# Kernel optimization log

Hardware: AMD Instinct MI355X
Metric: run time of the kernel (lower is better)

Reference implementation:

```python
import jax, jax.numpy as jnp
import numpy as np


def setup_inputs() -> dict:
    key = jax.random.key(0)
    ks = jax.random.split(key, 12)
    B, D, H, T, K = 12288, 1024, 512, 12, 3
    s = 0.02  # weight init scale for numerical stability
    return {
        "x": jax.random.normal(ks[0], (B, D), jnp.float32),
        "Wp": jax.random.normal(ks[1], (H, D), jnp.float32) * s,
        "bp": jnp.zeros((H,), jnp.float32),
        "opW1": jax.random.normal(ks[2], (T, K, H, H), jnp.float32) * s,
        "opb1": jnp.zeros((T, K, H), jnp.float32),
        "opW2": jax.random.normal(ks[3], (T, K, H, H), jnp.float32) * s,
        "opb2": jnp.zeros((T, K, H), jnp.float32),
        "op_logits": jax.random.normal(ks[4], (T, K), jnp.float32) * 0.1,
        "id_emb": jax.random.normal(ks[5], (T, 4), jnp.float32),
        "rW1": jax.random.normal(ks[6], (H, H + 7), jnp.float32) * s,
        "rb1": jnp.zeros((H,), jnp.float32),
        "rW2": jax.random.normal(ks[7], (T + 1, H), jnp.float32) * s,
        "rb2": jnp.zeros((T + 1,), jnp.float32),
        "gW1": jax.random.normal(ks[8], (T, H, 7), jnp.float32) * s,
        "gb1": jnp.zeros((T, H), jnp.float32),
        "gW2": jax.random.normal(ks[9], (T, 2, H), jnp.float32) * s,
        "gb2": jnp.zeros((T, 2), jnp.float32),
        "phW": jax.random.normal(ks[10], (D, H), jnp.float32) * s,
        "phb": jnp.zeros((D,), jnp.float32),
        "noise": jax.random.normal(ks[11], (B, H), jnp.float32),
    }


def reference(x, Wp, bp, opW1, opb1, opW2, opb2, op_logits, id_emb,
              rW1, rb1, rW2, rb2, gW1, gb1, gW2, gb2, phW, phb, noise):
    T, K, H, _ = opW1.shape
    B = x.shape[0]
    g = B // T  # balanced deterministic routing: patch p -> temper p % T

    # input projection (patch_size == hidden_dim => patches == x_proj)
    xp = x @ Wp.T + bp                                   # [B, H]
    xg = xp.reshape(g, T, H).transpose(1, 0, 2)           # [T, g, H]

    # Temper.apply_operators: softmax-weighted sum of Linear-ReLU-Linear-ReLU ops
    w = jax.nn.softmax(op_logits, axis=-1)                # [T, K]
    h1 = jax.nn.relu(jnp.einsum('tgj,tkij->tkgi', xg, opW1) + opb1[:, :, None, :])
    h2 = jax.nn.relu(jnp.einsum('tkgj,tkij->tkgi', h1, opW2) + opb2[:, :, None, :])
    out = jnp.einsum('tk,tkgi->tgi', w, h2)               # [T, g, H]
    # freshness buffers start at 0 -> fresh-bonus branch inactive

    usage = w                                             # usage starts at 0, += w
    conflict = jnp.std(w, axis=-1, ddof=1)                # torch.std is unbiased
    plast_t = ((out - xg) ** 2).mean(axis=(1, 2))         # last_plasticity per temper

    # IntrinsicGrowthController.compute_intrinsic_signals (buffers at init values)
    ng = noise.reshape(g, T, H).transpose(1, 0, 2) * 0.01
    plasticity = (ng ** 2).mean(-1)                       # [T, g] ((out_noisy-out)^2)
    novelty = (xg ** 2).mean(-1)                          # input_mean == 0
    pred_err = ((out - xg) ** 2).mean(-1)
    up = usage / (usage.sum(-1, keepdims=True) + 1e-6)
    entropy = -(up * jnp.log(jnp.clip(up, 1e-6, None))).sum(-1)   # [T]
    sparsity = jnp.abs(out).mean(-1)
    reward_delta = -pred_err                              # moving avg starts at 0
    new_avg = 0.01 * pred_err.mean(-1)                    # updated moving avg
    reward_var = ((pred_err - new_avg[:, None]) ** 2).mean(-1)
    signals = jnp.stack([plasticity.mean(-1), novelty.mean(-1), pred_err.mean(-1),
                         entropy, sparsity.mean(-1), reward_delta.mean(-1),
                         reward_var], axis=-1)            # [T, 7]

    # growth controller MLP 7 -> H -> 2 (per temper)
    gc_h = jax.nn.relu(jnp.einsum('thj,tj->th', gW1, signals) + gb1)
    decision = jnp.einsum('toh,th->to', gW2, gc_h) + gb2  # [T, 2] (grow, prune)

    # enriched routing input: [out | id_embed(4) | novelty | conflict | plasticity]
    nov_e = jnp.broadcast_to(signals[:, 1][:, None, None], (T, g, 1))
    conf_e = jnp.broadcast_to(conflict[:, None, None], (T, g, 1))
    plas_e = jnp.broadcast_to(plast_t[:, None, None], (T, g, 1))
    ide = jnp.broadcast_to(id_emb[:, None, :], (T, g, id_emb.shape[1]))
    enriched = jnp.concatenate([out, ide, nov_e, conf_e, plas_e], axis=-1)  # [T,g,H+7]

    rh = jax.nn.relu(jnp.einsum('tgj,ij->tgi', enriched, rW1) + rb1)
    logits = jnp.einsum('tgj,ij->tgi', rh, rW2) + rb2     # [T, g, T+1]

    # scatter back to original patch order (inverse of the grouping reshape)
    out_full = out.transpose(1, 0, 2).reshape(B, H)
    logits_full = logits.transpose(1, 0, 2).reshape(B, T + 1)
    pred = out_full @ phW.T + phb                         # predictive head [B, D]
    return (out_full, logits_full, pred, decision)
```

## Files before the change

### kernel.cpp

```cpp
#include <hip/hip_runtime.h>

typedef unsigned short u16;
typedef float f32x4 __attribute__((ext_vector_type(4)));
typedef float f32x8 __attribute__((ext_vector_type(8)));
typedef u16   u16x4 __attribute__((ext_vector_type(4)));
typedef u16   u16x8 __attribute__((ext_vector_type(8)));
typedef __bf16 bf16x8 __attribute__((ext_vector_type(8)));

#define WS_W       0u
#define WS_BIASRH  512u
#define WS_WPB     25600u
#define WS_PHWB    1074176u
#define WS_RW1B    2122752u
#define WS_W1B     2647040u
#define WS_W2B     21521408u
#define WS_XPB     40395776u
#define WS_H1B     52978688u
#define WS_XBF     90727424u
#define WS_OUTB    90727424u
#define WS_RHB     103310336u

#define OUT_LG   6291456
#define OUT_PRED 6451200
#define OUT_DEC  19034112

__device__ __forceinline__ u16 f2bf(float f) {
    unsigned u = __builtin_bit_cast(unsigned, f);
    return (u16)((u + 0x7FFFu + ((u >> 16) & 1u)) >> 16);
}
__device__ __forceinline__ float bf2f(u16 h) {
    return __builtin_bit_cast(float, (unsigned)h << 16);
}

typedef __attribute__((address_space(1))) void* gas1p;
typedef __attribute__((address_space(3))) void* las3p;
__device__ __forceinline__ void gload16(const u16* g, u16* l) {
    __builtin_amdgcn_global_load_lds((gas1p)(unsigned long long)g,
                                     (las3p)(unsigned)(unsigned long long)l,
                                     16, 0, 0);
}

__device__ __forceinline__ void zero_acc(f32x4 (&a)[4][4]) {
#pragma unroll
    for (int i = 0; i < 4; i++)
#pragma unroll
        for (int j = 0; j < 4; j++)
            a[i][j] = (f32x4){0.f, 0.f, 0.f, 0.f};
}

__device__ __forceinline__ void mfma_loop(
    const u16* __restrict__ Ab, size_t pa,
    const u16* __restrict__ Bb, size_t pb,
    int K, u16* sA, u16* sB, f32x4 (&acc)[4][4])
{
    const int tid = threadIdx.x;
    const int l = tid & 63, wv = tid >> 6;
    const int wm = (wv >> 1) * 64, wn = (wv & 1) * 64;
    const int m16 = l & 15, k8 = l >> 4;
    const int kc = (tid & 3) * 8;
    const size_t ra0 = (size_t)(tid >> 2) * pa + kc;
    const size_t ra1 = ra0 + 64 * pa;
    const size_t rb0 = (size_t)(tid >> 2) * pb + kc;
    const size_t rb1 = rb0 + 64 * pb;
    u16* dA0 = sA + tid * 8;          u16* dA1 = sA + (tid + 256) * 8;
    u16* dB0 = sB + tid * 8;          u16* dB1 = sB + (tid + 256) * 8;
    const int aO = (wm + m16) * 32 + k8 * 8;
    const int bO = (wn + m16) * 32 + k8 * 8;
    for (int kt = 0; kt < K; kt += 32) {
        __syncthreads();
        gload16(Ab + ra0 + kt, dA0);
        gload16(Ab + ra1 + kt, dA1);
        gload16(Bb + rb0 + kt, dB0);
        gload16(Bb + rb1 + kt, dB1);
        __syncthreads();
        bf16x8 af[4], bv[4];
#pragma unroll
        for (int i = 0; i < 4; i++) af[i] = *(const bf16x8*)(sA + aO + i * 512);
#pragma unroll
        for (int i = 0; i < 4; i++) bv[i] = *(const bf16x8*)(sB + bO + i * 512);
#pragma unroll
        for (int i = 0; i < 4; i++)
#pragma unroll
            for (int j = 0; j < 4; j++)
                acc[i][j] = __builtin_amdgcn_mfma_f32_16x16x32_bf16(af[i], bv[j], acc[i][j], 0, 0, 0);
    }
}

__device__ __forceinline__ void mfma_loop64(
    const u16* __restrict__ Ab, size_t pa,
    const u16* __restrict__ Bb, size_t pb,
    int K, u16* sA, u16* sB, f32x4 (&acc)[4][2])
{
    const int tid = threadIdx.x;
    const int l = tid & 63, wv = tid >> 6;
    const int m16 = l & 15, k8 = l >> 4;
    const int kc = (tid & 3) * 8;
    const size_t ra0 = (size_t)(tid >> 2) * pa + kc;
    const size_t rb0 = (size_t)(tid >> 2) * pb + kc;
    const size_t rb1 = rb0 + 64 * pb;
    u16* dA0 = sA + tid * 8;
    u16* dB0 = sB + tid * 8;          u16* dB1 = sB + (tid + 256) * 8;
    const int aO = m16 * 32 + k8 * 8;
    const int bO = (wv * 32 + m16) * 32 + k8 * 8;
    for (int kt = 0; kt < K; kt += 32) {
        __syncthreads();
        gload16(Ab + ra0 + kt, dA0);
        gload16(Bb + rb0 + kt, dB0);
        gload16(Bb + rb1 + kt, dB1);
        __syncthreads();
        bf16x8 af[4], bv[2];
#pragma unroll
        for (int i = 0; i < 4; i++) af[i] = *(const bf16x8*)(sA + aO + i * 512);
#pragma unroll
        for (int j = 0; j < 2; j++) bv[j] = *(const bf16x8*)(sB + bO + j * 512);
#pragma unroll
        for (int i = 0; i < 4; i++)
#pragma unroll
            for (int j = 0; j < 2; j++)
                acc[i][j] = __builtin_amdgcn_mfma_f32_16x16x32_bf16(af[i], bv[j], acc[i][j], 0, 0, 0);
    }
}

__global__ __launch_bounds__(256) void cvt6(
    const float* __restrict__ opW1, u16* __restrict__ w1b,
    const float* __restrict__ opW2, u16* __restrict__ w2b,
    const float* __restrict__ Wp,   u16* __restrict__ wpb,
    const float* __restrict__ phW,  u16* __restrict__ phwb,
    const float* __restrict__ rW1,  u16* __restrict__ rw1b,
    const float* __restrict__ op_logits, float* __restrict__ wbuf)
{
    if (blockIdx.x == 0 && threadIdx.x < 12) {
        const int t = threadIdx.x;
        float l0 = op_logits[t*3+0], l1 = op_logits[t*3+1], l2 = op_logits[t*3+2];
        float mx = fmaxf(l0, fmaxf(l1, l2));
        float e0 = expf(l0-mx), e1 = expf(l1-mx), e2 = expf(l2-mx);
        float inv = 1.f / (e0 + e1 + e2);
        wbuf[t*3+0] = e0*inv; wbuf[t*3+1] = e1*inv; wbuf[t*3+2] = e2*inv;
    }
    int i = (blockIdx.x * 256 + threadIdx.x) * 4;
    const float* s; u16* d;
    if (i < 9437184)                    { s = opW1; d = w1b; }
    else if ((i -= 9437184) < 9437184)  { s = opW2; d = w2b; }
    else if ((i -= 9437184) < 524288)   { s = Wp;   d = wpb; }
    else if ((i -= 524288)  < 524288)   { s = phW;  d = phwb; }
    else {
        i -= 524288;
        int row = i >> 9, j = i & 511;
        const float* sr = rW1 + (size_t)row * 519 + j;
        u16x4 o = { f2bf(sr[0]), f2bf(sr[1]), f2bf(sr[2]), f2bf(sr[3]) };
        *(u16x4*)(rw1b + i) = o;
        return;
    }
    f32x4 v = *(const f32x4*)(s + i);
    u16x4 o = { f2bf(v[0]), f2bf(v[1]), f2bf(v[2]), f2bf(v[3]) };
    *(u16x4*)(d + i) = o;
}

__global__ __launch_bounds__(256) void kgemm_xp(
    const float* __restrict__ x, const u16* __restrict__ wpb,
    const float* __restrict__ bp, u16* __restrict__ xpb)
{
    __shared__ u16 sA[2048], sB[4096];
    const int rowBase = blockIdx.y * 64, colBase = blockIdx.x * 128;
    const int tid = threadIdx.x, l = tid & 63, wv = tid >> 6;
    const int m16 = l & 15, k8 = l >> 4;
    const int kc = (tid & 3) * 8;
    const float* xrow = x + (size_t)(rowBase + (tid >> 2)) * 1024 + kc;
    const u16* Bb = wpb + (size_t)colBase * 1024;
    const size_t rb0 = (size_t)(tid >> 2) * 1024 + kc;
    const size_t rb1 = rb0 + 64 * 1024;
    u16* dA = sA + tid * 8;
    u16* dB0 = sB + tid * 8;          u16* dB1 = sB + (tid + 256) * 8;
    const int aO = m16 * 32 + k8 * 8;
    const int bO = (wv * 32 + m16) * 32 + k8 * 8;
    f32x4 acc[4][2];
#pragma unroll
    for (int i = 0; i < 4; i++)
#pragma unroll
        for (int j = 0; j < 2; j++) acc[i][j] = (f32x4){0.f,0.f,0.f,0.f};
    for (int kt = 0; kt < 1024; kt += 32) {
        f32x8 av = *(const f32x8*)(xrow + kt);
        __syncthreads();
        gload16(Bb + rb0 + kt, dB0);
        gload16(Bb + rb1 + kt, dB1);
        u16x8 ac;
#pragma unroll
        for (int j = 0; j < 8; j++) ac[j] = f2bf(av[j]);
        *(u16x8*)dA = ac;
        __syncthreads();
        bf16x8 af[4], bv[2];
#pragma unroll
        for (int i = 0; i < 4; i++) af[i] = *(const bf16x8*)(sA + aO + i * 512);
#pragma unroll
        for (int j = 0; j < 2; j++) bv[j] = *(const bf16x8*)(sB + bO + j * 512);
#pragma unroll
        for (int i = 0; i < 4; i++)
#pragma unroll
            for (int j = 0; j < 2; j++)
                acc[i][j] = __builtin_amdgcn_mfma_f32_16x16x32_bf16(af[i], bv[j], acc[i][j], 0, 0, 0);
    }
#pragma unroll
    for (int in = 0; in < 2; in++) {
        const int gc = colBase + wv * 32 + in * 16 + m16;
        const float bv = bp[gc];
#pragma unroll
        for (int im = 0; im < 4; im++) {
            const int gr = rowBase + im * 16 + k8 * 4;
#pragma unroll
            for (int r = 0; r < 4; r++)
                xpb[(size_t)(gr + r) * 512 + gc] = f2bf(acc[im][in][r] + bv);
        }
    }
}

__global__ __launch_bounds__(256) void kgemm_h1(
    const u16* __restrict__ xpb, const u16* __restrict__ w1b,
    const float* __restrict__ opb1, u16* __restrict__ h1b)
{
    __shared__ u16 sA[4096], sB[4096];
    const int seg = blockIdx.z, t = seg / 3;
    const int rowBase = blockIdx.y * 128, colBase = blockIdx.x * 128;
    f32x4 acc[4][4]; zero_acc(acc);
    mfma_loop(xpb + (size_t)rowBase * 6144 + (size_t)t * 512, 6144,
              w1b + (size_t)seg * 262144 + (size_t)colBase * 512, 512, 512, sA, sB, acc);
    const int tid = threadIdx.x, l = tid & 63, wv = tid >> 6;
    const int wm = (wv >> 1) * 64, wn = (wv & 1) * 64, m16 = l & 15, k8 = l >> 4;
    u16* hseg = h1b + (size_t)seg * 524288;
#pragma unroll
    for (int in = 0; in < 4; in++) {
        const int gc = colBase + wn + in * 16 + m16;
        const float bv = opb1[seg * 512 + gc];
#pragma unroll
        for (int im = 0; im < 4; im++) {
            const int gr = rowBase + wm + im * 16 + k8 * 4;
#pragma unroll
            for (int r = 0; r < 4; r++)
                hseg[(size_t)(gr + r) * 512 + gc] = f2bf(fmaxf(acc[im][in][r] + bv, 0.f));
        }
    }
}

__global__ __launch_bounds__(256) void kgemm_out(
    const u16* __restrict__ h1b, const u16* __restrict__ w2b,
    const float* __restrict__ opb2, const float* __restrict__ wbuf,
    float* __restrict__ outF, u16* __restrict__ outb)
{
    __shared__ u16 sA[2048], sB[4096];
    const int t = blockIdx.z;
    const int rowBase = blockIdx.y * 64, colBase = blockIdx.x * 128;
    const int tid = threadIdx.x, l = tid & 63, wv = tid >> 6;
    const int m16 = l & 15, k8 = l >> 4;
    float oac[4][2][4];
#pragma unroll
    for (int i = 0; i < 4; i++)
#pragma unroll
        for (int j = 0; j < 2; j++)
#pragma unroll
            for (int r = 0; r < 4; r++) oac[i][j][r] = 0.f;

    for (int kk = 0; kk < 3; kk++) {
        const int seg = t * 3 + kk;
        f32x4 acc[4][2];
#pragma unroll
        for (int i = 0; i < 4; i++)
#pragma unroll
            for (int j = 0; j < 2; j++) acc[i][j] = (f32x4){0.f,0.f,0.f,0.f};
        mfma_loop64(h1b + ((size_t)seg * 1024 + rowBase) * 512, 512,
                    w2b + (size_t)seg * 262144 + (size_t)colBase * 512, 512, 512, sA, sB, acc);
        const float wk = wbuf[seg];
#pragma unroll
        for (int in = 0; in < 2; in++) {
            const float bv = opb2[seg * 512 + colBase + wv * 32 + in * 16 + m16];
#pragma unroll
            for (int im = 0; im < 4; im++)
#pragma unroll
                for (int r = 0; r < 4; r++)
                    oac[im][in][r] += wk * fmaxf(acc[im][in][r] + bv, 0.f);
        }
    }
#pragma unroll
    for (int im = 0; im < 4; im++)
#pragma unroll
        for (int r = 0; r < 4; r++) {
            const int gi = rowBase + im * 16 + k8 * 4 + r;
            const size_t b = (size_t)gi * 12 + t;
#pragma unroll
            for (int in = 0; in < 2; in++) {
                const int gc = colBase + wv * 32 + in * 16 + m16;
                const float v = oac[im][in][r];
                outF[b * 512 + gc] = v;
                outb[b * 512 + gc] = f2bf(v);
            }
        }
}

__global__ __launch_bounds__(256) void kgemm_predrh(
    const u16* __restrict__ outb, const u16* __restrict__ phwb,
    const float* __restrict__ phb, const u16* __restrict__ rw1b,
    const float* __restrict__ bias_rh, float* __restrict__ outPred,
    u16* __restrict__ rhb)
{
    __shared__ u16 sA[4096], sB[4096];
    const int bz = blockIdx.x;
    const int rowBase = blockIdx.y * 128;
    const bool isPred = bz < 8;
    const int colBase = (isPred ? bz : bz - 8) * 128;
    const u16* Bb = isPred ? (phwb + (size_t)colBase * 512)
                           : (rw1b + (size_t)colBase * 512);
    f32x4 acc[4][4]; zero_acc(acc);
    mfma_loop(outb + (size_t)rowBase * 512, 512, Bb, 512, 512, sA, sB, acc);
    const int tid = threadIdx.x, l = tid & 63, wv = tid >> 6;
    const int wm = (wv >> 1) * 64, wn = (wv & 1) * 64, m16 = l & 15, k8 = l >> 4;
    if (isPred) {
#pragma unroll
        for (int in = 0; in < 4; in++) {
            const int gc = colBase + wn + in * 16 + m16;
            const float bv = phb[gc];
#pragma unroll
            for (int im = 0; im < 4; im++) {
                const int gr = rowBase + wm + im * 16 + k8 * 4;
#pragma unroll
                for (int r = 0; r < 4; r++)
                    outPred[(size_t)(gr + r) * 1024 + gc] = acc[im][in][r] + bv;
            }
        }
    } else {
#pragma unroll
        for (int in = 0; in < 4; in++) {
            const int gc = colBase + wn + in * 16 + m16;
#pragma unroll
            for (int im = 0; im < 4; im++) {
                const int gr = rowBase + wm + im * 16 + k8 * 4;
#pragma unroll
                for (int r = 0; r < 4; r++) {
                    const int b = gr + r;
                    const float bv = bias_rh[(b % 12) * 512 + gc];
                    rhb[(size_t)b * 512 + gc] = f2bf(fmaxf(acc[im][in][r] + bv, 0.f));
                }
            }
        }
    }
}

__global__ __launch_bounds__(256) void rowred(
    const float* __restrict__ outF, const u16* __restrict__ xpb,
    const float* __restrict__ noise, float* __restrict__ partials)
{
    const int tid = threadIdx.x, l = tid & 63, wv = tid >> 6;
    const int gw = blockIdx.x * 4 + wv;
    const size_t base = (size_t)gw * 12 * 512 + l * 8;
    float* pout = partials + (size_t)gw * 60;
#pragma unroll
    for (int t = 0; t < 12; t++) {
        const size_t off = base + (size_t)t * 512;
        f32x8 ov = *(const f32x8*)(outF + off);
        f32x8 nv = *(const f32x8*)(noise + off);
        u16x8 xv = *(const u16x8*)(xpb + off);
        float s1 = 0, s2 = 0, s3 = 0, s4 = 0;
#pragma unroll
        for (int j = 0; j < 8; j++) {
            float xg = bf2f(xv[j]);
            float o = ov[j];
            float d = o - xg;
            s1 += d * d; s2 += xg * xg; s3 += fabsf(o); s4 += nv[j] * nv[j];
        }
#pragma unroll
        for (int off2 = 32; off2 > 0; off2 >>= 1) {
            s1 += __shfl_xor(s1, off2);
            s2 += __shfl_xor(s2, off2);
            s3 += __shfl_xor(s3, off2);
            s4 += __shfl_xor(s4, off2);
        }
        if (l < 5) {
            float v = (l == 0) ? s1 : (l == 1) ? s2 : (l == 2) ? s3
                    : (l == 3) ? s4 : s1 * s1;
            pout[t * 5 + l] = v;
        }
    }
}

__global__ __launch_bounds__(256) void sig_kernel(
    const float* __restrict__ op_logits, const float* __restrict__ id_emb,
    const float* __restrict__ rW1, const float* __restrict__ rb1,
    const float* __restrict__ gW1, const float* __restrict__ gb1,
    const float* __restrict__ gW2, const float* __restrict__ gb2,
    const float* __restrict__ partials, float* __restrict__ bias_rh,
    float* __restrict__ outDec)
{
    const int t = blockIdx.x, tid = threadIdx.x;
    __shared__ float sig[7], ex7[7], gch[512], red[256], accv[5];
    float a[5] = {0.f, 0.f, 0.f, 0.f, 0.f};
    for (int g = tid; g < 1024; g += 256) {
        const float* p = partials + (size_t)g * 60 + t * 5;
#pragma unroll
        for (int s = 0; s < 5; s++) a[s] += p[s];
    }
#pragma unroll
    for (int s = 0; s < 5; s++) {
        red[tid] = a[s]; __syncthreads();
        for (int k = 128; k > 0; k >>= 1) { if (tid < k) red[tid] += red[tid + k]; __syncthreads(); }
        if (tid == 0) accv[s] = red[0];
        __syncthreads();
    }
    if (tid == 0) {
        float l0 = op_logits[t*3+0], l1 = op_logits[t*3+1], l2 = op_logits[t*3+2];
        float mx = fmaxf(l0, fmaxf(l1, l2));
        float e0 = expf(l0-mx), e1 = expf(l1-mx), e2 = expf(l2-mx);
        float es = e0 + e1 + e2;
        float w0 = e0/es, w1 = e1/es, w2 = e2/es;
        float mean = (w0 + w1 + w2) * (1.f/3.f);
        float var = ((w0-mean)*(w0-mean) + (w1-mean)*(w1-mean) + (w2-mean)*(w2-mean)) * 0.5f;
        float conflict = sqrtf(var);
        float inv_s = 1.f / (w0 + w1 + w2 + 1e-6f);
        float u0 = w0*inv_s, u1 = w1*inv_s, u2 = w2*inv_s;
        float ent = -(u0*logf(fmaxf(u0,1e-6f)) + u1*logf(fmaxf(u1,1e-6f)) + u2*logf(fmaxf(u2,1e-6f)));
        const float inv = 1.f / (1024.f * 512.f);
        float plast = accv[0] * inv;
        float nov   = accv[1] * inv;
        float spars = accv[2] * inv;
        float plasticity = 1e-4f * accv[3] * inv;
        float pe2 = accv[4] * (1.f / (1024.f * 512.f * 512.f));
        float na = 0.01f * plast;
        float rvar = pe2 - 2.f*na*plast + na*na;
        sig[0]=plasticity; sig[1]=nov; sig[2]=plast; sig[3]=ent; sig[4]=spars; sig[5]=-plast; sig[6]=rvar;
        ex7[0]=id_emb[t*4+0]; ex7[1]=id_emb[t*4+1]; ex7[2]=id_emb[t*4+2]; ex7[3]=id_emb[t*4+3];
        ex7[4]=nov; ex7[5]=conflict; ex7[6]=plast;
    }
    __syncthreads();
    for (int h = tid; h < 512; h += 256) {
        float aa = gb1[t*512 + h];
#pragma unroll
        for (int j = 0; j < 7; j++) aa += gW1[(t*512 + h)*7 + j] * sig[j];
        gch[h] = fmaxf(aa, 0.f);
        float bb = rb1[h];
#pragma unroll
        for (int e = 0; e < 7; e++) bb += ex7[e] * rW1[(size_t)h * 519 + 512 + e];
        bias_rh[t*512 + h] = bb;
    }
    __syncthreads();
    float p0 = 0.f, p1 = 0.f;
    for (int h = tid; h < 512; h += 256) {
        p0 += gW2[(t*2 + 0)*512 + h] * gch[h];
        p1 += gW2[(t*2 + 1)*512 + h] * gch[h];
    }
    red[tid] = p0; __syncthreads();
    for (int s = 128; s > 0; s >>= 1) { if (tid < s) red[tid] += red[tid + s]; __syncthreads(); }
    if (tid == 0) outDec[t*2 + 0] = red[0] + gb2[t*2 + 0];
    __syncthreads();
    red[tid] = p1; __syncthreads();
    for (int s = 128; s > 0; s >>= 1) { if (tid < s) red[tid] += red[tid + s]; __syncthreads(); }
    if (tid == 0) outDec[t*2 + 1] = red[0] + gb2[t*2 + 1];
}

__global__ __launch_bounds__(256) void logits_kernel(
    const u16* __restrict__ rhb, const float* __restrict__ rW2,
    const float* __restrict__ rb2, float* __restrict__ outLg)
{
    __shared__ float T2[512 * 13];
    __shared__ float rb2s[16];
    const int tid = threadIdx.x;
    for (int i = tid; i < 6656; i += 256) {
        int o = i >> 9, j = i & 511;
        T2[j * 13 + o] = rW2[i];
    }
    if (tid < 13) rb2s[tid] = rb2[tid];
    __syncthreads();
    const int l = tid & 63, wv = tid >> 6;
    const size_t b = (size_t)blockIdx.x * 4 + wv;
    const u16* rrow = rhb + b * 512;
    float rv[8];
#pragma unroll
    for (int jj = 0; jj < 8; jj++) rv[jj] = bf2f(rrow[l + 64 * jj]);
    float p[13];
#pragma unroll
    for (int o = 0; o < 13; o++) p[o] = 0.f;
#pragma unroll
    for (int jj = 0; jj < 8; jj++) {
        const float* tp = T2 + (l + 64 * jj) * 13;
#pragma unroll
        for (int o = 0; o < 13; o++) p[o] += rv[jj] * tp[o];
    }
#pragma unroll
    for (int o = 0; o < 13; o++) {
#pragma unroll
        for (int off = 32; off > 0; off >>= 1) p[o] += __shfl_xor(p[o], off);
    }
    if (l == 0) {
        float* orow = outLg + b * 13;
#pragma unroll
        for (int o = 0; o < 13; o++) orow[o] = p[o] + rb2s[o];
    }
}

extern "C" void kernel_launch(void* const* d_in, const int* in_sizes, int n_in,
                              void* d_out, int out_size, void* d_ws, size_t ws_size,
                              hipStream_t stream)
{
    const float* x         = (const float*)d_in[0];
    const float* Wp        = (const float*)d_in[1];
    const float* bp        = (const float*)d_in[2];
    const float* opW1      = (const float*)d_in[3];
    const float* opb1      = (const float*)d_in[4];
    const float* opW2      = (const float*)d_in[5];
    const float* opb2      = (const float*)d_in[6];
    const float* op_logits = (const float*)d_in[7];
    const float* id_emb    = (const float*)d_in[8];
    const float* rW1       = (const float*)d_in[9];
    const float* rb1       = (const float*)d_in[10];
    const float* rW2       = (const float*)d_in[11];
    const float* rb2       = (const float*)d_in[12];
    const float* gW1       = (const float*)d_in[13];
    const float* gb1       = (const float*)d_in[14];
    const float* gW2       = (const float*)d_in[15];
    const float* gb2       = (const float*)d_in[16];
    const float* phW       = (const float*)d_in[17];
    const float* phb       = (const float*)d_in[18];
    const float* noise     = (const float*)d_in[19];

    char* ws = (char*)d_ws;
    float* wbuf    = (float*)(ws + WS_W);
    float* bias_rh = (float*)(ws + WS_BIASRH);
    u16* wpb  = (u16*)(ws + WS_WPB);
    u16* phwb = (u16*)(ws + WS_PHWB);
    u16* rw1b = (u16*)(ws + WS_RW1B);
    u16* w1b  = (u16*)(ws + WS_W1B);
    u16* w2b  = (u16*)(ws + WS_W2B);
    u16* xpb  = (u16*)(ws + WS_XPB);
    u16* h1b  = (u16*)(ws + WS_H1B);
    u16* outb = (u16*)(ws + WS_OUTB);
    u16* rhb  = (u16*)(ws + WS_RHB);
    float* partials = (float*)(ws + WS_W1B);

    float* outF    = (float*)d_out;
    float* outLg   = outF + OUT_LG;
    float* outPred = outF + OUT_PRED;
    float* outDec  = outF + OUT_DEC;

    cvt6<<<19712, 256, 0, stream>>>(opW1, w1b, opW2, w2b, Wp, wpb,
                                    phW, phwb, rW1, rw1b, op_logits, wbuf);
    kgemm_xp  <<<dim3(4, 192),    256, 0, stream>>>(x, wpb, bp, xpb);
    kgemm_h1  <<<dim3(4, 8, 36),  256, 0, stream>>>(xpb, w1b, opb1, h1b);
    kgemm_out <<<dim3(4, 16, 12), 256, 0, stream>>>(h1b, w2b, opb2, wbuf, outF, outb);
    rowred    <<<256,             256, 0, stream>>>(outF, xpb, noise, partials);
    sig_kernel<<<12,              256, 0, stream>>>(op_logits, id_emb, rW1, rb1, gW1, gb1,
                                                    gW2, gb2, partials, bias_rh, outDec);
    kgemm_predrh<<<dim3(12, 96),  256, 0, stream>>>(outb, phwb, phb, rw1b, bias_rh,
                                                    outPred, rhb);
    logits_kernel<<<3072,         256, 0, stream>>>(rhb, rW2, rb2, outLg);
}
```

Before: 410.6 us.

## Double-buffer LDS tiles in MFMA GEMM loops to overlap loads with compute

Converts the shared-memory tiling in all GEMM mainloops to a two-stage ping-pong buffer. The next K-slice is prefetched via global-to-LDS loads while the current one is consumed, with explicit vmcnt waits and raw s_barrier in place of paired __syncthreads. The xp kernel also prefetches its fp32 x row into registers one step ahead before converting it to bf16. LDS usage doubles per block, which may lower occupancy, and the hand-written waitcnt values must match the number of outstanding loads exactly.

```diff
diff --git a/kernel.cpp b/kernel.cpp
--- a/kernel.cpp
+++ b/kernel.cpp
@@ -16,7 +16,6 @@
 #define WS_W2B     21521408u
 #define WS_XPB     40395776u
 #define WS_H1B     52978688u
-#define WS_XBF     90727424u
 #define WS_OUTB    90727424u
 #define WS_RHB     103310336u
 
@@ -62,27 +61,40 @@
     const size_t ra1 = ra0 + 64 * pa;
     const size_t rb0 = (size_t)(tid >> 2) * pb + kc;
     const size_t rb1 = rb0 + 64 * pb;
-    u16* dA0 = sA + tid * 8;          u16* dA1 = sA + (tid + 256) * 8;
-    u16* dB0 = sB + tid * 8;          u16* dB1 = sB + (tid + 256) * 8;
     const int aO = (wm + m16) * 32 + k8 * 8;
     const int bO = (wn + m16) * 32 + k8 * 8;
+    gload16(Ab + ra0, sA + tid * 8);
+    gload16(Ab + ra1, sA + (tid + 256) * 8);
+    gload16(Bb + rb0, sB + tid * 8);
+    gload16(Bb + rb1, sB + (tid + 256) * 8);
+    int cur = 0;
     for (int kt = 0; kt < K; kt += 32) {
-        __syncthreads();
-        gload16(Ab + ra0 + kt, dA0);
-        gload16(Ab + ra1 + kt, dA1);
-        gload16(Bb + rb0 + kt, dB0);
-        gload16(Bb + rb1 + kt, dB1);
-        __syncthreads();
+        __builtin_amdgcn_s_barrier();
+        const int nx = cur ^ 1;
+        if (kt + 32 < K) {
+            const int kn = kt + 32;
+            gload16(Ab + ra0 + kn, sA + nx * 4096 + tid * 8);
+            gload16(Ab + ra1 + kn, sA + nx * 4096 + (tid + 256) * 8);
+            gload16(Bb + rb0 + kn, sB + nx * 4096 + tid * 8);
+            gload16(Bb + rb1 + kn, sB + nx * 4096 + (tid + 256) * 8);
+            asm volatile("s_waitcnt vmcnt(4)" ::: "memory");
+        } else {
+            asm volatile("s_waitcnt vmcnt(0)" ::: "memory");
+        }
+        __builtin_amdgcn_s_barrier();
+        const u16* cA = sA + cur * 4096;
+        const u16* cB = sB + cur * 4096;
         bf16x8 af[4], bv[4];
 #pragma unroll
-        for (int i = 0; i < 4; i++) af[i] = *(const bf16x8*)(sA + aO + i * 512);
-#pragma unroll
-        for (int i = 0; i < 4; i++) bv[i] = *(const bf16x8*)(sB + bO + i * 512);
+        for (int i = 0; i < 4; i++) af[i] = *(const bf16x8*)(cA + aO + i * 512);
+#pragma unroll
+        for (int i = 0; i < 4; i++) bv[i] = *(const bf16x8*)(cB + bO + i * 512);
 #pragma unroll
         for (int i = 0; i < 4; i++)
 #pragma unroll
             for (int j = 0; j < 4; j++)
                 acc[i][j] = __builtin_amdgcn_mfma_f32_16x16x32_bf16(af[i], bv[j], acc[i][j], 0, 0, 0);
+        cur = nx;
     }
 }
 
@@ -98,26 +110,38 @@
     const size_t ra0 = (size_t)(tid >> 2) * pa + kc;
     const size_t rb0 = (size_t)(tid >> 2) * pb + kc;
     const size_t rb1 = rb0 + 64 * pb;
-    u16* dA0 = sA + tid * 8;
-    u16* dB0 = sB + tid * 8;          u16* dB1 = sB + (tid + 256) * 8;
     const int aO = m16 * 32 + k8 * 8;
     const int bO = (wv * 32 + m16) * 32 + k8 * 8;
+    gload16(Ab + ra0, sA + tid * 8);
+    gload16(Bb + rb0, sB + tid * 8);
+    gload16(Bb + rb1, sB + (tid + 256) * 8);
+    int cur = 0;
     for (int kt = 0; kt < K; kt += 32) {
-        __syncthreads();
-        gload16(Ab + ra0 + kt, dA0);
-        gload16(Bb + rb0 + kt, dB0);
-        gload16(Bb + rb1 + kt, dB1);
-        __syncthreads();
+        __builtin_amdgcn_s_barrier();
+        const int nx = cur ^ 1;
+        if (kt + 32 < K) {
+            const int kn = kt + 32;
+            gload16(Ab + ra0 + kn, sA + nx * 2048 + tid * 8);
+            gload16(Bb + rb0 + kn, sB + nx * 4096 + tid * 8);
+            gload16(Bb + rb1 + kn, sB + nx * 4096 + (tid + 256) * 8);
+            asm volatile("s_waitcnt vmcnt(3)" ::: "memory");
+        } else {
+            asm volatile("s_waitcnt vmcnt(0)" ::: "memory");
+        }
+        __builtin_amdgcn_s_barrier();
+        const u16* cA = sA + cur * 2048;
+        const u16* cB = sB + cur * 4096;
         bf16x8 af[4], bv[2];
 #pragma unroll
-        for (int i = 0; i < 4; i++) af[i] = *(const bf16x8*)(sA + aO + i * 512);
-#pragma unroll
-        for (int j = 0; j < 2; j++) bv[j] = *(const bf16x8*)(sB + bO + j * 512);
+        for (int i = 0; i < 4; i++) af[i] = *(const bf16x8*)(cA + aO + i * 512);
+#pragma unroll
+        for (int j = 0; j < 2; j++) bv[j] = *(const bf16x8*)(cB + bO + j * 512);
 #pragma unroll
         for (int i = 0; i < 4; i++)
 #pragma unroll
             for (int j = 0; j < 2; j++)
                 acc[i][j] = __builtin_amdgcn_mfma_f32_16x16x32_bf16(af[i], bv[j], acc[i][j], 0, 0, 0);
+        cur = nx;
     }
 }
 
@@ -160,7 +184,7 @@
     const float* __restrict__ x, const u16* __restrict__ wpb,
     const float* __restrict__ bp, u16* __restrict__ xpb)
 {
-    __shared__ u16 sA[2048], sB[4096];
+    __shared__ u16 sA[4096], sB[8192];
     const int rowBase = blockIdx.y * 64, colBase = blockIdx.x * 128;
     const int tid = threadIdx.x, l = tid & 63, wv = tid >> 6;
     const int m16 = l & 15, k8 = l >> 4;
@@ -169,8 +193,6 @@
     const u16* Bb = wpb + (size_t)colBase * 1024;
     const size_t rb0 = (size_t)(tid >> 2) * 1024 + kc;
     const size_t rb1 = rb0 + 64 * 1024;
-    u16* dA = sA + tid * 8;
-    u16* dB0 = sB + tid * 8;          u16* dB1 = sB + (tid + 256) * 8;
     const int aO = m16 * 32 + k8 * 8;
     const int bO = (wv * 32 + m16) * 32 + k8 * 8;
     f32x4 acc[4][2];
@@ -178,26 +200,49 @@
     for (int i = 0; i < 4; i++)
 #pragma unroll
         for (int j = 0; j < 2; j++) acc[i][j] = (f32x4){0.f,0.f,0.f,0.f};
+
+    gload16(Bb + rb0, sB + tid * 8);
+    gload16(Bb + rb1, sB + (tid + 256) * 8);
+    {
+        f32x8 a0 = *(const f32x8*)(xrow);
+        u16x8 c;
+#pragma unroll
+        for (int j = 0; j < 8; j++) c[j] = f2bf(a0[j]);
+        *(u16x8*)(sA + tid * 8) = c;
+    }
+    f32x8 avR = *(const f32x8*)(xrow + 32);
+    asm volatile("s_waitcnt lgkmcnt(0)" ::: "memory");
+
+    int cur = 0;
     for (int kt = 0; kt < 1024; kt += 32) {
-        f32x8 av = *(const f32x8*)(xrow + kt);
-        __syncthreads();
-        gload16(Bb + rb0 + kt, dB0);
-        gload16(Bb + rb1 + kt, dB1);
-        u16x8 ac;
-#pragma unroll
-        for (int j = 0; j < 8; j++) ac[j] = f2bf(av[j]);
-        *(u16x8*)dA = ac;
-        __syncthreads();
+        __builtin_amdgcn_s_barrier();
+        const int nx = cur ^ 1;
+        if (kt + 32 < 1024) {
+            gload16(Bb + rb0 + kt + 32, sB + nx * 4096 + tid * 8);
+            gload16(Bb + rb1 + kt + 32, sB + nx * 4096 + (tid + 256) * 8);
+            u16x8 c;
+#pragma unroll
+            for (int j = 0; j < 8; j++) c[j] = f2bf(avR[j]);
+            *(u16x8*)(sA + nx * 2048 + tid * 8) = c;
+            avR = *(const f32x8*)(xrow + ((kt + 64) & 1023));
+            asm volatile("s_waitcnt lgkmcnt(0)" ::: "memory");
+        } else {
+            asm volatile("s_waitcnt vmcnt(0) lgkmcnt(0)" ::: "memory");
+        }
+        __builtin_amdgcn_s_barrier();
+        const u16* cA = sA + cur * 2048;
+        const u16* cB = sB + cur * 4096;
         bf16x8 af[4], bv[2];
 #pragma unroll
-        for (int i = 0; i < 4; i++) af[i] = *(const bf16x8*)(sA + aO + i * 512);
-#pragma unroll
-        for (int j = 0; j < 2; j++) bv[j] = *(const bf16x8*)(sB + bO + j * 512);
+        for (int i = 0; i < 4; i++) af[i] = *(const bf16x8*)(cA + aO + i * 512);
+#pragma unroll
+        for (int j = 0; j < 2; j++) bv[j] = *(const bf16x8*)(cB + bO + j * 512);
 #pragma unroll
         for (int i = 0; i < 4; i++)
 #pragma unroll
             for (int j = 0; j < 2; j++)
                 acc[i][j] = __builtin_amdgcn_mfma_f32_16x16x32_bf16(af[i], bv[j], acc[i][j], 0, 0, 0);
+        cur = nx;
     }
 #pragma unroll
     for (int in = 0; in < 2; in++) {
@@ -217,7 +262,7 @@
     const u16* __restrict__ xpb, const u16* __restrict__ w1b,
     const float* __restrict__ opb1, u16* __restrict__ h1b)
 {
-    __shared__ u16 sA[4096], sB[4096];
+    __shared__ u16 sA[8192], sB[8192];
     const int seg = blockIdx.z, t = seg / 3;
     const int rowBase = blockIdx.y * 128, colBase = blockIdx.x * 128;
     f32x4 acc[4][4]; zero_acc(acc);
@@ -245,7 +290,7 @@
     const float* __restrict__ opb2, const float* __restrict__ wbuf,
     float* __restrict__ outF, u16* __restrict__ outb)
 {
-    __shared__ u16 sA[2048], sB[4096];
+    __shared__ u16 sA[4096], sB[8192];
     const int t = blockIdx.z;
     const int rowBase = blockIdx.y * 64, colBase = blockIdx.x * 128;
     const int tid = threadIdx.x, l = tid & 63, wv = tid >> 6;
@@ -300,7 +345,7 @@
     const float* __restrict__ bias_rh, float* __restrict__ outPred,
     u16* __restrict__ rhb)
 {
-    __shared__ u16 sA[4096], sB[4096];
+    __shared__ u16 sA[8192], sB[8192];
     const int bz = blockIdx.x;
     const int rowBase = blockIdx.y * 128;
     const bool isPred = bz < 8;
```

After: 398.0 us. 3.1% less time.
